# Performance work log

Hardware: AMD Instinct MI355X
Metric: run time of the kernel (lower is better)

## Reference

```python
import jax, jax.numpy as jnp
import numpy as np

B, S, HID, DK, DV, H = 4, 2048, 1024, 1024, 1024, 16
NEG = -1e9


def setup_inputs() -> dict:
    key = jax.random.key(0)
    ks = jax.random.split(key, 7)
    sc = HID ** -0.5
    queries = jax.random.normal(ks[0], (B, S, HID), jnp.float32)
    keys_ = jax.random.normal(ks[1], (B, S, HID), jnp.float32)
    values = jax.random.normal(ks[2], (B, S, HID), jnp.float32)
    Wq = jax.random.normal(ks[3], (HID, DK), jnp.float32) * sc
    Wk = jax.random.normal(ks[4], (HID, DK), jnp.float32) * sc
    Wv = jax.random.normal(ks[5], (HID, DV), jnp.float32) * sc
    Wo = jax.random.normal(ks[6], (DV, HID), jnp.float32) * sc
    # additive causal mask buffer [1,1,S,S]: -1e9 above diagonal
    mask = jnp.where(jnp.tril(jnp.ones((S, S), jnp.bool_)), 0.0, NEG).astype(jnp.float32)[None, None]
    return {"queries": queries, "keys": keys_, "values": values, "mask": mask,
            "Wq": Wq, "Wk": Wk, "Wv": Wv, "Wo": Wo}


def reference(queries, keys, values, mask, Wq, Wk, Wv, Wo):
    scale = (DK // H) ** -0.5
    q = jnp.einsum('bsd,de->bse', queries, Wq)
    k = jnp.einsum('bsd,de->bse', keys, Wk)
    v = jnp.einsum('bsd,de->bse', values, Wv)
    # split heads -> [B, H, S, head_dim]
    q = q.reshape(B, S, H, DK // H).transpose(0, 2, 1, 3) * scale
    k = k.reshape(B, S, H, DK // H).transpose(0, 2, 1, 3)
    v = v.reshape(B, S, H, DV // H).transpose(0, 2, 1, 3)
    logits = jnp.einsum('bhqd,bhkd->bhqk', q, k) + mask[:, :, :S, :S]
    weights = jax.nn.softmax(logits, axis=-1)  # dropout p=0 (eval)
    ctx = jnp.einsum('bhqk,bhkd->bhqd', weights, v)
    ctx = ctx.transpose(0, 2, 1, 3).reshape(B, S, DV)
    return jnp.einsum('bsd,de->bse', ctx, Wo)
```

## Files before the change

### kernel.cpp

```cpp
#include <hip/hip_runtime.h>

typedef __bf16 bf16_t;
typedef __bf16 bf16x4 __attribute__((ext_vector_type(4)));
typedef __bf16 bf16x8 __attribute__((ext_vector_type(8)));
typedef float f32x4 __attribute__((ext_vector_type(4)));
typedef float f32x4v __attribute__((ext_vector_type(4)));

#define GLOAD_LDS16(gptr, lptr) \
  __builtin_amdgcn_global_load_lds((const __attribute__((address_space(1))) void*)(gptr), \
                                   (__attribute__((address_space(3))) void*)(lptr), 16, 0, 0)


__global__ __launch_bounds__(256) void cast_x_kernel(
    const float* __restrict__ q, const float* __restrict__ k,
    const float* __restrict__ v, bf16_t* __restrict__ out) {
  const int z = blockIdx.y;
  const float* src = (z == 0) ? q : (z == 1) ? k : v;
  size_t i = ((size_t)blockIdx.x * 256 + threadIdx.x) * 4;
  f32x4v val = *(const f32x4v*)(src + i);
  bf16x4 o;
  o[0] = (bf16_t)val[0]; o[1] = (bf16_t)val[1];
  o[2] = (bf16_t)val[2]; o[3] = (bf16_t)val[3];
  *(bf16x4*)(out + (size_t)z * 8388608 + i) = o;
}

__global__ __launch_bounds__(256) void cast_w_kernel(
    const float* __restrict__ W0, const float* __restrict__ W1,
    const float* __restrict__ W2, const float* __restrict__ W3,
    bf16_t* __restrict__ Wt) {
  const int z = blockIdx.z;
  const float* W = (z == 0) ? W0 : (z == 1) ? W1 : (z == 2) ? W2 : W3;
  const float sc = (z == 0) ? 0.18033688011112042f : 1.0f;
  __shared__ float tile[64][65];
  const int n0 = blockIdx.x * 64, k0 = blockIdx.y * 64;
  const int t = threadIdx.x;
  const int r = t >> 4, c4 = (t & 15) * 4;
#pragma unroll
  for (int p = 0; p < 4; p++) {
    f32x4v v = *(const f32x4v*)&W[(size_t)(k0 + r + p * 16) * 1024 + n0 + c4];
    tile[r + p * 16][c4 + 0] = v[0]; tile[r + p * 16][c4 + 1] = v[1];
    tile[r + p * 16][c4 + 2] = v[2]; tile[r + p * 16][c4 + 3] = v[3];
  }
  __syncthreads();
  const int r2 = t >> 3, c2 = (t & 7) * 8;
  bf16_t* dst = Wt + (size_t)z * 1048576;
#pragma unroll
  for (int p = 0; p < 2; p++) {
    bf16x8 o;
#pragma unroll
    for (int i = 0; i < 8; i++) o[i] = (bf16_t)(tile[c2 + i][r2 + p * 32] * sc);
    *(bf16x8*)&dst[(size_t)(n0 + r2 + p * 32) * 1024 + k0 + c2] = o;
  }
}

template <int EPI>
__global__ __launch_bounds__(256) void gemm_bt(
    const bf16_t* __restrict__ Abase, const bf16_t* __restrict__ Wtbase,
    void* __restrict__ outp) {
  __shared__ bf16_t As[128 * 32];
  __shared__ bf16_t Bs[128 * 32];
  const int mt = blockIdx.x, nt = blockIdx.y, z = blockIdx.z;
  const int tid = threadIdx.x, wave = tid >> 6, lane = tid & 63;
  const bf16_t* A = Abase + (size_t)z * 8388608 + (size_t)mt * 128 * 1024;
  const bf16_t* Bt = Wtbase + (size_t)z * 1048576 + (size_t)nt * 128 * 1024;

  const int wm = wave >> 1, wn = wave & 1;
  const int frow = lane & 15, fk = (lane >> 4) * 8;
  const int srow = lane >> 2, scol = (lane & 3) * 8;

  f32x4 acc[4][4];
#pragma unroll
  for (int i = 0; i < 4; i++)
#pragma unroll
    for (int j = 0; j < 4; j++) acc[i][j] = (f32x4){0.f, 0.f, 0.f, 0.f};

  for (int k0 = 0; k0 < 1024; k0 += 32) {
#pragma unroll
    for (int r = 0; r < 2; r++) {
      const int c = wave * 2 + r;
      GLOAD_LDS16(A + (size_t)(c * 16 + srow) * 1024 + k0 + scol, &As[c * 512]);
      GLOAD_LDS16(Bt + (size_t)(c * 16 + srow) * 1024 + k0 + scol, &Bs[c * 512]);
    }
    __syncthreads();
    bf16x8 af[4], bfr[4];
#pragma unroll
    for (int i = 0; i < 4; i++)
      af[i] = *(const bf16x8*)&As[(wm * 64 + i * 16 + frow) * 32 + fk];
#pragma unroll
    for (int j = 0; j < 4; j++)
      bfr[j] = *(const bf16x8*)&Bs[(wn * 64 + j * 16 + frow) * 32 + fk];
#pragma unroll
    for (int i = 0; i < 4; i++)
#pragma unroll
      for (int j = 0; j < 4; j++)
        acc[i][j] = __builtin_amdgcn_mfma_f32_16x16x32_bf16(af[i], bfr[j],
                                                            acc[i][j], 0, 0, 0);
    __syncthreads();
  }

  const int rbase = mt * 128 + wm * 64;
  if constexpr (EPI == 0) {
    bf16_t* out = (bf16_t*)outp + (size_t)z * 8388608;
    const int h = nt * 2 + wn;
#pragma unroll
    for (int i = 0; i < 4; i++)
#pragma unroll
      for (int j = 0; j < 4; j++)
#pragma unroll
        for (int r = 0; r < 4; r++) {
          int row_g = rbase + i * 16 + (lane >> 4) * 4 + r;
          int b = row_g >> 11, s = row_g & 2047;
          int dd = j * 16 + frow;
          out[(((size_t)(b * 16 + h)) * 2048 + s) * 64 + dd] = (bf16_t)acc[i][j][r];
        }
  } else {
    float* out = (float*)outp;
#pragma unroll
    for (int i = 0; i < 4; i++)
#pragma unroll
      for (int j = 0; j < 4; j++)
#pragma unroll
        for (int r = 0; r < 4; r++) {
          int row_g = rbase + i * 16 + (lane >> 4) * 4 + r;
          int col_g = nt * 128 + wn * 64 + j * 16 + frow;
          out[(size_t)row_g * 1024 + col_g] = acc[i][j][r];
        }
  }
}

__global__ __launch_bounds__(256) void attn_fwd(const bf16_t* __restrict__ qkv,
                                                bf16_t* __restrict__ ctx) {
  const int bh = blockIdx.x;
  const int y = blockIdx.y;
  const int b = bh >> 4, h = bh & 15;
  const size_t HS = (size_t)2048 * 64;
  const bf16_t* Qp = qkv + (size_t)bh * HS;
  const bf16_t* Kp = qkv + 8388608 + (size_t)bh * HS;
  const bf16_t* Vp = qkv + 16777216 + (size_t)bh * HS;

  __shared__ bf16_t Klds[64 * 72];
  __shared__ bf16_t VT[64 * 68];

  const int tid = threadIdx.x, wave = tid >> 6, lane = tid & 63;
  const int q15 = lane & 15, g = lane >> 4;

#pragma unroll 1
  for (int s = 0; s < 2; s++) {
    const int qt = s ? (15 - y) : y;
    const int qbase = qt * 128 + wave * 32;
    const int nkv = qt * 2 + 2;
    const int qmax = qbase + 31;

    bf16x8 qf[2][2];
#pragma unroll
    for (int mf = 0; mf < 2; mf++)
#pragma unroll
      for (int kf = 0; kf < 2; kf++)
        qf[mf][kf] = *(const bf16x8*)&Qp[(size_t)(qbase + mf * 16 + q15) * 64 +
                                         kf * 32 + g * 8];

    float m[2] = {-1e30f, -1e30f}, l[2] = {0.f, 0.f};
    f32x4 of[2][4];
#pragma unroll
    for (int mf = 0; mf < 2; mf++)
#pragma unroll
      for (int nd = 0; nd < 4; nd++) of[mf][nd] = (f32x4){0.f, 0.f, 0.f, 0.f};

    for (int kv = 0; kv < nkv; ++kv) {
      const int kv0 = kv * 64;
      bf16x8 kreg[2], vreg[2];
#pragma unroll
      for (int p = 0; p < 2; p++) {
        int id = tid + p * 256;
        int row = id >> 3, col = (id & 7) * 8;
        kreg[p] = *(const bf16x8*)&Kp[(size_t)(kv0 + row) * 64 + col];
        vreg[p] = *(const bf16x8*)&Vp[(size_t)(kv0 + row) * 64 + col];
      }
      __syncthreads();
#pragma unroll
      for (int p = 0; p < 2; p++) {
        int id = tid + p * 256;
        int row = id >> 3, col = (id & 7) * 8;
        *(bf16x8*)&Klds[row * 72 + col] = kreg[p];
        const int swz8 = col;
#pragma unroll
        for (int i = 0; i < 8; i++)
          VT[(col + i) * 68 + (row ^ (swz8 & 56))] = vreg[p][i];
      }
      __syncthreads();

      if (kv0 > qmax) continue;

      f32x4 sf[2][4];
#pragma unroll
      for (int nf = 0; nf < 4; nf++) {
        bf16x8 ka = *(const bf16x8*)&Klds[(nf * 16 + q15) * 72 + g * 8];
        bf16x8 kb = *(const bf16x8*)&Klds[(nf * 16 + q15) * 72 + 32 + g * 8];
#pragma unroll
        for (int mf = 0; mf < 2; mf++) {
          f32x4 a = (f32x4){0.f, 0.f, 0.f, 0.f};
          a = __builtin_amdgcn_mfma_f32_16x16x32_bf16(ka, qf[mf][0], a, 0, 0, 0);
          a = __builtin_amdgcn_mfma_f32_16x16x32_bf16(kb, qf[mf][1], a, 0, 0, 0);
          sf[mf][nf] = a;
        }
      }

      if (kv >= 2 * qt + (wave >> 1)) {
#pragma unroll
        for (int mf = 0; mf < 2; mf++) {
          int q_g = qbase + mf * 16 + q15;
#pragma unroll
          for (int nf = 0; nf < 4; nf++)
#pragma unroll
            for (int r = 0; r < 4; r++)
              if (kv0 + nf * 16 + g * 4 + r > q_g) sf[mf][nf][r] = -1e30f;
        }
      }

      bf16x8 ap[2][2];
#pragma unroll
      for (int mf = 0; mf < 2; mf++) {
        float pmax = sf[mf][0][0];
#pragma unroll
        for (int nf = 0; nf < 4; nf++)
#pragma unroll
          for (int r = 0; r < 4; r++) pmax = fmaxf(pmax, sf[mf][nf][r]);
        pmax = fmaxf(pmax, __shfl_xor(pmax, 16));
        pmax = fmaxf(pmax, __shfl_xor(pmax, 32));
        float mold = m[mf];
        if (!__all(pmax <= mold + 8.0f)) {
          float mnew = fmaxf(mold, pmax);
          float alpha = __builtin_amdgcn_exp2f(mold - mnew);
          m[mf] = mnew;
          l[mf] *= alpha;
#pragma unroll
          for (int r = 0; r < 4; r++) {
            float aO = __shfl(alpha, (lane & 48) | (g * 4 + r));
#pragma unroll
            for (int nd = 0; nd < 4; nd++) of[mf][nd][r] *= aO;
          }
        }
        float mm = m[mf];
        float rs = 0.f;
#pragma unroll
        for (int nf = 0; nf < 4; nf++)
#pragma unroll
          for (int r = 0; r < 4; r++) {
            float pp = __builtin_amdgcn_exp2f(sf[mf][nf][r] - mm);
            sf[mf][nf][r] = pp;
            rs += pp;
          }
        rs += __shfl_xor(rs, 16);
        rs += __shfl_xor(rs, 32);
        l[mf] += rs;
#pragma unroll
        for (int kf = 0; kf < 2; kf++)
#pragma unroll
          for (int j2 = 0; j2 < 4; j2++) {
            ap[mf][kf][j2] = (bf16_t)sf[mf][2 * kf][j2];
            ap[mf][kf][j2 + 4] = (bf16_t)sf[mf][2 * kf + 1][j2];
          }
      }

#pragma unroll
      for (int nd = 0; nd < 4; nd++) {
        const int d = nd * 16 + q15;
        const int swz8 = (d >> 3 & 7) * 8;
#pragma unroll
        for (int kf = 0; kf < 2; kf++) {
          bf16x4 v0 = *(const bf16x4*)&VT[d * 68 + ((kf * 32 + 4 * g) ^ swz8)];
          bf16x4 v1 = *(const bf16x4*)&VT[d * 68 + ((kf * 32 + 16 + 4 * g) ^ swz8)];
          bf16x8 vv;
#pragma unroll
          for (int i = 0; i < 4; i++) { vv[i] = v0[i]; vv[i + 4] = v1[i]; }
#pragma unroll
          for (int mf = 0; mf < 2; mf++)
            of[mf][nd] = __builtin_amdgcn_mfma_f32_16x16x32_bf16(ap[mf][kf], vv,
                                                                 of[mf][nd], 0, 0, 0);
        }
      }
    }

#pragma unroll
    for (int mf = 0; mf < 2; mf++) {
      float rcpO[4];
#pragma unroll
      for (int r = 0; r < 4; r++) {
        float lO = __shfl(l[mf], (lane & 48) | (g * 4 + r));
        rcpO[r] = 1.0f / lO;
      }
#pragma unroll
      for (int nd = 0; nd < 4; nd++)
#pragma unroll
        for (int r = 0; r < 4; r++) {
          int srow_ = qbase + mf * 16 + g * 4 + r;
          ctx[((size_t)(b * 2048 + srow_)) * 1024 + h * 64 + nd * 16 + q15] =
              (bf16_t)(of[mf][nd][r] * rcpO[r]);
        }
    }
  }
}


extern "C" void kernel_launch(void* const* d_in, const int* in_sizes, int n_in,
                              void* d_out, int out_size, void* d_ws, size_t ws_size,
                              hipStream_t stream) {
  const float* queries = (const float*)d_in[0];
  const float* keys    = (const float*)d_in[1];
  const float* values  = (const float*)d_in[2];
  const float* Wq = (const float*)d_in[4];
  const float* Wk = (const float*)d_in[5];
  const float* Wv = (const float*)d_in[6];
  const float* Wo = (const float*)d_in[7];

  char* ws = (char*)d_ws;
  bf16_t* Xb  = (bf16_t*)ws;
  bf16_t* qkv = (bf16_t*)(ws + 50331648);
  bf16_t* Wt  = (bf16_t*)(ws + 100663296);
  bf16_t* ctx = Xb;
  float* out = (float*)d_out;

  cast_x_kernel<<<dim3(8192, 3), 256, 0, stream>>>(queries, keys, values, Xb);
  cast_w_kernel<<<dim3(16, 16, 4), 256, 0, stream>>>(Wq, Wk, Wv, Wo, Wt);
  gemm_bt<0><<<dim3(64, 8, 3), 256, 0, stream>>>(Xb, Wt, (void*)qkv);
  attn_fwd<<<dim3(64, 8), 256, 0, stream>>>(qkv, ctx);
  gemm_bt<1><<<dim3(64, 8, 1), 256, 0, stream>>>(ctx, Wt + 3 * 1048576, (void*)out);
}
```

Before: 189.4 us.

## Use eight waves of 16 query rows each in attention kernel

The attention kernel goes from 4 waves with 32 query rows each to 8 waves with 16 rows each, so blocks have 512 threads. Each thread now loads a single K/V chunk per tile, and the causal-mask check is done per wave based on its 16-row range. This roughly doubles the number of waves per block to improve latency hiding and lets more waves skip masked or empty tiles. In exchange, each K fragment read from LDS feeds only one MFMA instead of two, and the K/V staging cost is spread over more waves.

```diff
diff --git a/kernel.cpp b/kernel.cpp
--- a/kernel.cpp
+++ b/kernel.cpp
@@ -128,7 +128,7 @@
   }
 }
 
-__global__ __launch_bounds__(256) void attn_fwd(const bf16_t* __restrict__ qkv,
+__global__ __launch_bounds__(512) void attn_fwd(const bf16_t* __restrict__ qkv,
                                                 bf16_t* __restrict__ ctx) {
   const int bh = blockIdx.x;
   const int y = blockIdx.y;
@@ -143,124 +143,99 @@
 
   const int tid = threadIdx.x, wave = tid >> 6, lane = tid & 63;
   const int q15 = lane & 15, g = lane >> 4;
+  const int ldrow = tid >> 3, ldcol = (tid & 7) * 8;
 
 #pragma unroll 1
   for (int s = 0; s < 2; s++) {
     const int qt = s ? (15 - y) : y;
-    const int qbase = qt * 128 + wave * 32;
+    const int qbase = qt * 128 + wave * 16;
     const int nkv = qt * 2 + 2;
-    const int qmax = qbase + 31;
-
-    bf16x8 qf[2][2];
-#pragma unroll
-    for (int mf = 0; mf < 2; mf++)
-#pragma unroll
-      for (int kf = 0; kf < 2; kf++)
-        qf[mf][kf] = *(const bf16x8*)&Qp[(size_t)(qbase + mf * 16 + q15) * 64 +
-                                         kf * 32 + g * 8];
-
-    float m[2] = {-1e30f, -1e30f}, l[2] = {0.f, 0.f};
-    f32x4 of[2][4];
-#pragma unroll
-    for (int mf = 0; mf < 2; mf++)
-#pragma unroll
-      for (int nd = 0; nd < 4; nd++) of[mf][nd] = (f32x4){0.f, 0.f, 0.f, 0.f};
+    const int qmax = qbase + 15;
+
+    bf16x8 qf[2];
+#pragma unroll
+    for (int kf = 0; kf < 2; kf++)
+      qf[kf] = *(const bf16x8*)&Qp[(size_t)(qbase + q15) * 64 + kf * 32 + g * 8];
+
+    float m = -1e30f, l = 0.f;
+    f32x4 of[4];
+#pragma unroll
+    for (int nd = 0; nd < 4; nd++) of[nd] = (f32x4){0.f, 0.f, 0.f, 0.f};
 
     for (int kv = 0; kv < nkv; ++kv) {
       const int kv0 = kv * 64;
-      bf16x8 kreg[2], vreg[2];
-#pragma unroll
-      for (int p = 0; p < 2; p++) {
-        int id = tid + p * 256;
-        int row = id >> 3, col = (id & 7) * 8;
-        kreg[p] = *(const bf16x8*)&Kp[(size_t)(kv0 + row) * 64 + col];
-        vreg[p] = *(const bf16x8*)&Vp[(size_t)(kv0 + row) * 64 + col];
-      }
+      bf16x8 kreg = *(const bf16x8*)&Kp[(size_t)(kv0 + ldrow) * 64 + ldcol];
+      bf16x8 vreg = *(const bf16x8*)&Vp[(size_t)(kv0 + ldrow) * 64 + ldcol];
       __syncthreads();
-#pragma unroll
-      for (int p = 0; p < 2; p++) {
-        int id = tid + p * 256;
-        int row = id >> 3, col = (id & 7) * 8;
-        *(bf16x8*)&Klds[row * 72 + col] = kreg[p];
-        const int swz8 = col;
-#pragma unroll
-        for (int i = 0; i < 8; i++)
-          VT[(col + i) * 68 + (row ^ (swz8 & 56))] = vreg[p][i];
-      }
+      *(bf16x8*)&Klds[ldrow * 72 + ldcol] = kreg;
+#pragma unroll
+      for (int i = 0; i < 8; i++)
+        VT[(ldcol + i) * 68 + (ldrow ^ (ldcol & 56))] = vreg[i];
       __syncthreads();
 
       if (kv0 > qmax) continue;
 
-      f32x4 sf[2][4];
+      f32x4 sf[4];
 #pragma unroll
       for (int nf = 0; nf < 4; nf++) {
         bf16x8 ka = *(const bf16x8*)&Klds[(nf * 16 + q15) * 72 + g * 8];
         bf16x8 kb = *(const bf16x8*)&Klds[(nf * 16 + q15) * 72 + 32 + g * 8];
-#pragma unroll
-        for (int mf = 0; mf < 2; mf++) {
-          f32x4 a = (f32x4){0.f, 0.f, 0.f, 0.f};
-          a = __builtin_amdgcn_mfma_f32_16x16x32_bf16(ka, qf[mf][0], a, 0, 0, 0);
-          a = __builtin_amdgcn_mfma_f32_16x16x32_bf16(kb, qf[mf][1], a, 0, 0, 0);
-          sf[mf][nf] = a;
-        }
-      }
-
-      if (kv >= 2 * qt + (wave >> 1)) {
-#pragma unroll
-        for (int mf = 0; mf < 2; mf++) {
-          int q_g = qbase + mf * 16 + q15;
-#pragma unroll
-          for (int nf = 0; nf < 4; nf++)
-#pragma unroll
-            for (int r = 0; r < 4; r++)
-              if (kv0 + nf * 16 + g * 4 + r > q_g) sf[mf][nf][r] = -1e30f;
-        }
-      }
-
-      bf16x8 ap[2][2];
-#pragma unroll
-      for (int mf = 0; mf < 2; mf++) {
-        float pmax = sf[mf][0][0];
+        f32x4 a = (f32x4){0.f, 0.f, 0.f, 0.f};
+        a = __builtin_amdgcn_mfma_f32_16x16x32_bf16(ka, qf[0], a, 0, 0, 0);
+        a = __builtin_amdgcn_mfma_f32_16x16x32_bf16(kb, qf[1], a, 0, 0, 0);
+        sf[nf] = a;
+      }
+
+      if (kv0 + 63 > qbase) {
+        int q_g = qbase + q15;
 #pragma unroll
         for (int nf = 0; nf < 4; nf++)
 #pragma unroll
-          for (int r = 0; r < 4; r++) pmax = fmaxf(pmax, sf[mf][nf][r]);
-        pmax = fmaxf(pmax, __shfl_xor(pmax, 16));
-        pmax = fmaxf(pmax, __shfl_xor(pmax, 32));
-        float mold = m[mf];
-        if (!__all(pmax <= mold + 8.0f)) {
-          float mnew = fmaxf(mold, pmax);
-          float alpha = __builtin_amdgcn_exp2f(mold - mnew);
-          m[mf] = mnew;
-          l[mf] *= alpha;
-#pragma unroll
-          for (int r = 0; r < 4; r++) {
-            float aO = __shfl(alpha, (lane & 48) | (g * 4 + r));
-#pragma unroll
-            for (int nd = 0; nd < 4; nd++) of[mf][nd][r] *= aO;
-          }
-        }
-        float mm = m[mf];
-        float rs = 0.f;
-#pragma unroll
-        for (int nf = 0; nf < 4; nf++)
-#pragma unroll
-          for (int r = 0; r < 4; r++) {
-            float pp = __builtin_amdgcn_exp2f(sf[mf][nf][r] - mm);
-            sf[mf][nf][r] = pp;
-            rs += pp;
-          }
-        rs += __shfl_xor(rs, 16);
-        rs += __shfl_xor(rs, 32);
-        l[mf] += rs;
-#pragma unroll
-        for (int kf = 0; kf < 2; kf++)
-#pragma unroll
-          for (int j2 = 0; j2 < 4; j2++) {
-            ap[mf][kf][j2] = (bf16_t)sf[mf][2 * kf][j2];
-            ap[mf][kf][j2 + 4] = (bf16_t)sf[mf][2 * kf + 1][j2];
-          }
-      }
+          for (int r = 0; r < 4; r++)
+            if (kv0 + nf * 16 + g * 4 + r > q_g) sf[nf][r] = -1e30f;
+      }
+
+      float pmax = sf[0][0];
+#pragma unroll
+      for (int nf = 0; nf < 4; nf++)
+#pragma unroll
+        for (int r = 0; r < 4; r++) pmax = fmaxf(pmax, sf[nf][r]);
+      pmax = fmaxf(pmax, __shfl_xor(pmax, 16));
+      pmax = fmaxf(pmax, __shfl_xor(pmax, 32));
+      float mold = m;
+      if (!__all(pmax <= mold + 8.0f)) {
+        float mnew = fmaxf(mold, pmax);
+        float alpha = __builtin_amdgcn_exp2f(mold - mnew);
+        m = mnew;
+        l *= alpha;
+#pragma unroll
+        for (int r = 0; r < 4; r++) {
+          float aO = __shfl(alpha, (lane & 48) | (g * 4 + r));
+#pragma unroll
+          for (int nd = 0; nd < 4; nd++) of[nd][r] *= aO;
+        }
+      }
+      float mm = m;
+      float rs = 0.f;
+#pragma unroll
+      for (int nf = 0; nf < 4; nf++)
+#pragma unroll
+        for (int r = 0; r < 4; r++) {
+          float pp = __builtin_amdgcn_exp2f(sf[nf][r] - mm);
+          sf[nf][r] = pp;
+          rs += pp;
+        }
+      rs += __shfl_xor(rs, 16);
+      rs += __shfl_xor(rs, 32);
+      l += rs;
+      bf16x8 ap[2];
+#pragma unroll
+      for (int kf = 0; kf < 2; kf++)
+#pragma unroll
+        for (int j2 = 0; j2 < 4; j2++) {
+          ap[kf][j2] = (bf16_t)sf[2 * kf][j2];
+          ap[kf][j2 + 4] = (bf16_t)sf[2 * kf + 1][j2];
+        }
 
 #pragma unroll
       for (int nd = 0; nd < 4; nd++) {
@@ -273,31 +248,26 @@
           bf16x8 vv;
 #pragma unroll
           for (int i = 0; i < 4; i++) { vv[i] = v0[i]; vv[i + 4] = v1[i]; }
-#pragma unroll
-          for (int mf = 0; mf < 2; mf++)
-            of[mf][nd] = __builtin_amdgcn_mfma_f32_16x16x32_bf16(ap[mf][kf], vv,
-                                                                 of[mf][nd], 0, 0, 0);
+          of[nd] = __builtin_amdgcn_mfma_f32_16x16x32_bf16(ap[kf], vv,
+                                                           of[nd], 0, 0, 0);
         }
       }
     }
 
-#pragma unroll
-    for (int mf = 0; mf < 2; mf++) {
-      float rcpO[4];
+    float rcpO[4];
+#pragma unroll
+    for (int r = 0; r < 4; r++) {
+      float lO = __shfl(l, (lane & 48) | (g * 4 + r));
+      rcpO[r] = 1.0f / lO;
+    }
+#pragma unroll
+    for (int nd = 0; nd < 4; nd++)
 #pragma unroll
       for (int r = 0; r < 4; r++) {
-        float lO = __shfl(l[mf], (lane & 48) | (g * 4 + r));
-        rcpO[r] = 1.0f / lO;
-      }
-#pragma unroll
-      for (int nd = 0; nd < 4; nd++)
-#pragma unroll
-        for (int r = 0; r < 4; r++) {
-          int srow_ = qbase + mf * 16 + g * 4 + r;
-          ctx[((size_t)(b * 2048 + srow_)) * 1024 + h * 64 + nd * 16 + q15] =
-              (bf16_t)(of[mf][nd][r] * rcpO[r]);
-        }
-    }
+        int srow_ = qbase + g * 4 + r;
+        ctx[((size_t)(b * 2048 + srow_)) * 1024 + h * 64 + nd * 16 + q15] =
+            (bf16_t)(of[nd][r] * rcpO[r]);
+      }
   }
 }
 
@@ -323,6 +293,6 @@
   cast_x_kernel<<<dim3(8192, 3), 256, 0, stream>>>(queries, keys, values, Xb);
   cast_w_kernel<<<dim3(16, 16, 4), 256, 0, stream>>>(Wq, Wk, Wv, Wo, Wt);
   gemm_bt<0><<<dim3(64, 8, 3), 256, 0, stream>>>(Xb, Wt, (void*)qkv);
-  attn_fwd<<<dim3(64, 8), 256, 0, stream>>>(qkv, ctx);
+  attn_fwd<<<dim3(64, 8), 512, 0, stream>>>(qkv, ctx);
   gemm_bt<1><<<dim3(64, 8, 1), 256, 0, stream>>>(ctx, Wt + 3 * 1048576, (void*)out);
 }
```

Result: faster. 183.7 us (-3.0%).
